# Performance work log

Measured on AMD Instinct MI355X. Metric: run time of the kernel, lower is better.

The kernel has to match this reference:

```python
import jax, jax.numpy as jnp
import numpy as np

N_SPK, N_UTT, D_EMB = 1024, 20, 512
COS_EPS = 1e-8   # torch F.cosine_similarity default eps
SIM_EPS = 1e-6   # added to cosine and inside the log, per original code


def setup_inputs() -> dict:
    key = jax.random.key(0)
    embeddings = jax.random.normal(key, (N_SPK, N_UTT, D_EMB), dtype=jnp.float32)
    w = jnp.asarray(10.0, dtype=jnp.float32)
    b = jnp.asarray(-5.0, dtype=jnp.float32)
    return {"embeddings": embeddings, "w": w, "b": b}


def reference(embeddings, w, b):
    N, M, D = embeddings.shape
    sums = embeddings.sum(axis=1)                       # [N, D]
    centroids = sums / M                                # [N, D] full centroids
    cent_excl = (sums[:, None, :] - embeddings) / (M - 1)  # [N, M, D] leave-one-out

    def _norm(x):
        return x / jnp.maximum(jnp.linalg.norm(x, axis=-1, keepdims=True), COS_EPS)

    e_n = _norm(embeddings)          # [N, M, D]
    c_n = _norm(centroids)           # [N, D]
    ce_n = _norm(cent_excl)          # [N, M, D]

    # cosine vs every speaker centroid
    cs = jnp.einsum('nmd,kd->nmk', e_n, c_n)            # [N, M, N]
    # replace same-speaker column with leave-one-out cosine
    diag = jnp.sum(e_n * ce_n, axis=-1)                 # [N, M]
    same = jnp.eye(N, dtype=bool)[:, None, :]           # [N, 1, N]
    cossim = jnp.where(same, diag[:, :, None], cs) + SIM_EPS

    sim = w * cossim + b                                # [N, M, N]
    pos = w * (diag + SIM_EPS) + b                      # sim[j, i, j]
    lse = jnp.log(jnp.sum(jnp.exp(sim), axis=-1) + SIM_EPS)  # [N, M]
    loss = jnp.sum(lse - pos)
    return loss
```

## Files before the change

### kernel.cpp

```cpp
#include <hip/hip_runtime.h>
#include <hip/hip_bf16.h>

typedef unsigned short u16;
typedef unsigned int u32;
typedef __bf16 bf16x8 __attribute__((ext_vector_type(8)));
typedef float f32x4 __attribute__((ext_vector_type(4)));

#define NSPK 1024
#define NUTT 20
#define DEMB 512
#define NROW (NSPK * NUTT)

__device__ __forceinline__ u16 f2bf(float x) {
    union { float f; u32 u; } v; v.f = x;
    u32 r = (v.u + 0x7fffu + ((v.u >> 16) & 1u)) >> 16;
    return (u16)r;
}

__global__ __launch_bounds__(256) void prep_f(const float* __restrict__ E,
                                              u16* __restrict__ A,
                                              u16* __restrict__ Bc,
                                              float* __restrict__ diag,
                                              float* __restrict__ csd,
                                              float* __restrict__ rs,
                                              float* __restrict__ out) {
    __shared__ float sbuf[4][DEMB];
    const int t = threadIdx.x, lane = t & 63, wv = t >> 6;
    const int n = blockIdx.x;
    const float* Eb = E + (size_t)n * (NUTT * DEMB) + (size_t)(wv * 5) * DEMB + lane * 8;

    float4 e0[5], e1[5];
    float4 p0 = {0, 0, 0, 0}, p1 = {0, 0, 0, 0};
#pragma unroll
    for (int i = 0; i < 5; ++i) {
        e0[i] = *(const float4*)(Eb + (size_t)i * DEMB);
        e1[i] = *(const float4*)(Eb + (size_t)i * DEMB + 4);
        p0.x += e0[i].x; p0.y += e0[i].y; p0.z += e0[i].z; p0.w += e0[i].w;
        p1.x += e1[i].x; p1.y += e1[i].y; p1.z += e1[i].z; p1.w += e1[i].w;
    }
    *(float4*)(&sbuf[wv][lane * 8])     = p0;
    *(float4*)(&sbuf[wv][lane * 8 + 4]) = p1;
    __syncthreads();

    float4 s0 = {0, 0, 0, 0}, s1 = {0, 0, 0, 0};
#pragma unroll
    for (int k = 0; k < 4; ++k) {
        float4 a = *(const float4*)(&sbuf[k][lane * 8]);
        float4 b = *(const float4*)(&sbuf[k][lane * 8 + 4]);
        s0.x += a.x; s0.y += a.y; s0.z += a.z; s0.w += a.w;
        s1.x += b.x; s1.y += b.y; s1.z += b.z; s1.w += b.w;
    }

    float ls = s0.x*s0.x + s0.y*s0.y + s0.z*s0.z + s0.w*s0.w
             + s1.x*s1.x + s1.y*s1.y + s1.z*s1.z + s1.w*s1.w;
#pragma unroll
    for (int o = 32; o; o >>= 1) ls += __shfl_xor(ls, o);
    const float ss = ls;
    const float rc = 1.0f / fmaxf(sqrtf(ss) * 0.05f, 1e-8f);
    const float g  = rc * 0.05f;

    union { u16 h[8]; uint4 q; } ck;
    ck.h[0] = f2bf(s0.x * g); ck.h[1] = f2bf(s0.y * g);
    ck.h[2] = f2bf(s0.z * g); ck.h[3] = f2bf(s0.w * g);
    ck.h[4] = f2bf(s1.x * g); ck.h[5] = f2bf(s1.y * g);
    ck.h[6] = f2bf(s1.z * g); ck.h[7] = f2bf(s1.w * g);
    ((uint4*)(Bc + (size_t)n * DEMB))[lane] = ck.q;

#pragma unroll
    for (int i = 0; i < 5; ++i) {
        float ee = e0[i].x*e0[i].x + e0[i].y*e0[i].y + e0[i].z*e0[i].z + e0[i].w*e0[i].w
                 + e1[i].x*e1[i].x + e1[i].y*e1[i].y + e1[i].z*e1[i].z + e1[i].w*e1[i].w;
        float es = e0[i].x*s0.x + e0[i].y*s0.y + e0[i].z*s0.z + e0[i].w*s0.w
                 + e1[i].x*s1.x + e1[i].y*s1.y + e1[i].z*s1.z + e1[i].w*s1.w;
#pragma unroll
        for (int o = 32; o; o >>= 1) { ee += __shfl_xor(ee, o); es += __shfl_xor(es, o); }

        const float rne = 1.0f / fmaxf(sqrtf(ee), 1e-8f);
        const float pxx = ss - 2.f * es + ee;
        const float dg  = (es - ee) * rne / fmaxf(sqrtf(pxx), 1.9e-7f);

        const int r = n * NUTT + wv * 5 + i;
        union { u16 h[8]; uint4 q; } pk;
        pk.h[0] = f2bf(e0[i].x * rne); pk.h[1] = f2bf(e0[i].y * rne);
        pk.h[2] = f2bf(e0[i].z * rne); pk.h[3] = f2bf(e0[i].w * rne);
        pk.h[4] = f2bf(e1[i].x * rne); pk.h[5] = f2bf(e1[i].y * rne);
        pk.h[6] = f2bf(e1[i].z * rne); pk.h[7] = f2bf(e1[i].w * rne);
        ((uint4*)(A + (size_t)r * DEMB))[lane] = pk.q;
        if (lane == 0) {
            diag[r] = dg;
            csd[r]  = es * g * rne;
        }
    }

    if (t < NUTT) rs[n * NUTT + t] = 0.f;
    if (n == 0 && t == 0) out[0] = 0.f;
}

__device__ __forceinline__ void async_copy16(const void* g, void* l) {
    __builtin_amdgcn_global_load_lds(
        (const __attribute__((address_space(1))) void*)g,
        (__attribute__((address_space(3))) void*)l, 16, 0, 0);
}

__global__ __launch_bounds__(256) void gemm_exp(const u16* __restrict__ A,
                                                const u16* __restrict__ Bc,
                                                const float* __restrict__ wp,
                                                const float* __restrict__ bp,
                                                float* __restrict__ rowsum) {
    __shared__ u16 As[128 * 64];
    __shared__ u16 Bs[128 * 64];
    const int t = threadIdx.x;
    const int lane = t & 63, wv = t >> 6;
    const int ml = lane & 15, q = lane >> 4;
    const int wm = wv >> 1, wn = wv & 1;
    const int tileM = blockIdx.x;
    const int tileN = blockIdx.y;

    const float w = *wp, bb = *bp;

    const u16* Ag = A + (size_t)tileM * 128 * DEMB;
    const u16* Bg = Bc + (size_t)tileN * 128 * DEMB;

    const u16* asrc[4]; const u16* bsrc[4]; u16* adst[4]; u16* bdst[4];
#pragma unroll
    for (int j = 0; j < 4; ++j) {
        const int c = t + 256 * j;
        const int r = c >> 3, kg = (c & 7) ^ (r & 7);
        asrc[j] = Ag + (size_t)r * DEMB + kg * 8;  adst[j] = As + c * 8;
        bsrc[j] = Bg + (size_t)r * DEMB + kg * 8;  bdst[j] = Bs + c * 8;
    }

    int aoff[2][4], boff[2][4];
#pragma unroll
    for (int i = 0; i < 4; ++i) {
        const int r = wm * 64 + i * 16 + ml;
        const int c = wn * 64 + i * 16 + ml;
#pragma unroll
        for (int h = 0; h < 2; ++h) {
            aoff[h][i] = r * 64 + ((((h << 2) | q) ^ (r & 7)) << 3);
            boff[h][i] = c * 64 + ((((h << 2) | q) ^ (c & 7)) << 3);
        }
    }

    f32x4 acc[4][4];
#pragma unroll
    for (int i = 0; i < 4; ++i)
#pragma unroll
        for (int j = 0; j < 4; ++j) acc[i][j] = (f32x4){0.f, 0.f, 0.f, 0.f};

    for (int kt = 0; kt < DEMB; kt += 64) {
        __syncthreads();
#pragma unroll
        for (int j = 0; j < 4; ++j) async_copy16(asrc[j] + kt, adst[j]);
#pragma unroll
        for (int j = 0; j < 4; ++j) async_copy16(bsrc[j] + kt, bdst[j]);
        __syncthreads();

#pragma unroll
        for (int h = 0; h < 2; ++h) {
            bf16x8 af[4], bfv[4];
#pragma unroll
            for (int i = 0; i < 4; ++i) af[i]  = *(const bf16x8*)(As + aoff[h][i]);
#pragma unroll
            for (int j = 0; j < 4; ++j) bfv[j] = *(const bf16x8*)(Bs + boff[h][j]);
#pragma unroll
            for (int i = 0; i < 4; ++i)
#pragma unroll
                for (int j = 0; j < 4; ++j)
                    acc[i][j] = __builtin_amdgcn_mfma_f32_16x16x32_bf16(af[i], bfv[j], acc[i][j], 0, 0, 0);
        }
    }

#pragma unroll
    for (int i = 0; i < 4; ++i) {
        float s0 = 0.f, s1 = 0.f, s2 = 0.f, s3 = 0.f;
#pragma unroll
        for (int j = 0; j < 4; ++j) {
            s0 += __expf(fmaf(w, acc[i][j][0] + 1e-6f, bb));
            s1 += __expf(fmaf(w, acc[i][j][1] + 1e-6f, bb));
            s2 += __expf(fmaf(w, acc[i][j][2] + 1e-6f, bb));
            s3 += __expf(fmaf(w, acc[i][j][3] + 1e-6f, bb));
        }
#pragma unroll
        for (int o = 1; o < 16; o <<= 1) {
            s0 += __shfl_xor(s0, o); s1 += __shfl_xor(s1, o);
            s2 += __shfl_xor(s2, o); s3 += __shfl_xor(s3, o);
        }
        if (ml < 4) {
            float sv = (ml == 0) ? s0 : (ml == 1) ? s1 : (ml == 2) ? s2 : s3;
            int grow = tileM * 128 + wm * 64 + i * 16 + q * 4 + ml;
            atomicAdd(&rowsum[grow], sv);
        }
    }
}

__global__ __launch_bounds__(256) void finalize(const float* __restrict__ rowsum,
                                                const float* __restrict__ diag,
                                                const float* __restrict__ csd,
                                                const float* __restrict__ wp,
                                                const float* __restrict__ bp,
                                                float* __restrict__ out) {
    __shared__ float s_red[4];
    const int r = blockIdx.x * 256 + threadIdx.x;
    const float w = *wp, bb = *bp;
    const float dg = diag[r];
    const float pos = fmaf(w, dg + 1e-6f, bb);
    const float S = rowsum[r] - __expf(fmaf(w, csd[r] + 1e-6f, bb)) + __expf(pos);
    float term = logf(S + 1e-6f) - pos;
    const int lane = threadIdx.x & 63, wv = threadIdx.x >> 6;
#pragma unroll
    for (int o = 32; o; o >>= 1) term += __shfl_xor(term, o);
    if (lane == 0) s_red[wv] = term;
    __syncthreads();
    if (threadIdx.x == 0) atomicAdd(out, s_red[0] + s_red[1] + s_red[2] + s_red[3]);
}

extern "C" void kernel_launch(void* const* d_in, const int* in_sizes, int n_in,
                              void* d_out, int out_size, void* d_ws, size_t ws_size,
                              hipStream_t stream) {
    const float* E = (const float*)d_in[0];
    const float* wp = (const float*)d_in[1];
    const float* bp = (const float*)d_in[2];
    float* out = (float*)d_out;

    char* ws = (char*)d_ws;
    u16* A     = (u16*)(ws);
    u16* Bc    = (u16*)(ws + 20971520);
    float* dg  = (float*)(ws + 22020096);
    float* cs  = (float*)(ws + 22102016);
    float* rs  = (float*)(ws + 22183936);

    prep_f<<<NSPK, 256, 0, stream>>>(E, A, Bc, dg, cs, rs, out);
    gemm_exp<<<dim3(160, 8), 256, 0, stream>>>(A, Bc, wp, bp, rs);
    finalize<<<80, 256, 0, stream>>>(rs, dg, cs, wp, bp, out);
}
```

Baseline: 120.9 us.

## Switch similarity GEMM from bf16 to fp8 using scaled MFMA 16x16x128

Normalized embeddings and centroids are now quantized to fp8 instead of bf16, and the GEMM uses the MI355X scaled fp8 MFMA with a K=128 tile and unit scales. The goal is to halve the bytes written and loaded for A and B and to reach the higher fp8 matrix throughput. LDS tiles, swizzle offsets and workspace offsets are adjusted to match. The cost is much lower precision in the cosine values, which after scaling by w=10 and exponentiation may push the loss outside tolerance.

```diff
diff --git a/kernel.cpp b/kernel.cpp
--- a/kernel.cpp
+++ b/kernel.cpp
@@ -3,7 +3,8 @@
 
 typedef unsigned short u16;
 typedef unsigned int u32;
-typedef __bf16 bf16x8 __attribute__((ext_vector_type(8)));
+typedef unsigned char u8;
+typedef int i32x8 __attribute__((ext_vector_type(8)));
 typedef float f32x4 __attribute__((ext_vector_type(4)));
 
 #define NSPK 1024
@@ -11,15 +12,18 @@
 #define DEMB 512
 #define NROW (NSPK * NUTT)
 
-__device__ __forceinline__ u16 f2bf(float x) {
-    union { float f; u32 u; } v; v.f = x;
-    u32 r = (v.u + 0x7fffu + ((v.u >> 16) & 1u)) >> 16;
-    return (u16)r;
+__device__ __forceinline__ uint2 pk_fp8x8(float a, float b, float c, float d,
+                                          float e, float f, float g, float h) {
+    int lo = __builtin_amdgcn_cvt_pk_fp8_f32(a, b, 0, 0);
+    lo = __builtin_amdgcn_cvt_pk_fp8_f32(c, d, lo, 1);
+    int hi = __builtin_amdgcn_cvt_pk_fp8_f32(e, f, 0, 0);
+    hi = __builtin_amdgcn_cvt_pk_fp8_f32(g, h, hi, 1);
+    return make_uint2((u32)lo, (u32)hi);
 }
 
 __global__ __launch_bounds__(256) void prep_f(const float* __restrict__ E,
-                                              u16* __restrict__ A,
-                                              u16* __restrict__ Bc,
+                                              u8* __restrict__ A,
+                                              u8* __restrict__ Bc,
                                               float* __restrict__ diag,
                                               float* __restrict__ csd,
                                               float* __restrict__ rs,
@@ -59,12 +63,9 @@
     const float rc = 1.0f / fmaxf(sqrtf(ss) * 0.05f, 1e-8f);
     const float g  = rc * 0.05f;
 
-    union { u16 h[8]; uint4 q; } ck;
-    ck.h[0] = f2bf(s0.x * g); ck.h[1] = f2bf(s0.y * g);
-    ck.h[2] = f2bf(s0.z * g); ck.h[3] = f2bf(s0.w * g);
-    ck.h[4] = f2bf(s1.x * g); ck.h[5] = f2bf(s1.y * g);
-    ck.h[6] = f2bf(s1.z * g); ck.h[7] = f2bf(s1.w * g);
-    ((uint4*)(Bc + (size_t)n * DEMB))[lane] = ck.q;
+    ((uint2*)(Bc + (size_t)n * DEMB))[lane] =
+        pk_fp8x8(s0.x * g, s0.y * g, s0.z * g, s0.w * g,
+                 s1.x * g, s1.y * g, s1.z * g, s1.w * g);
 
 #pragma unroll
     for (int i = 0; i < 5; ++i) {
@@ -80,12 +81,9 @@
         const float dg  = (es - ee) * rne / fmaxf(sqrtf(pxx), 1.9e-7f);
 
         const int r = n * NUTT + wv * 5 + i;
-        union { u16 h[8]; uint4 q; } pk;
-        pk.h[0] = f2bf(e0[i].x * rne); pk.h[1] = f2bf(e0[i].y * rne);
-        pk.h[2] = f2bf(e0[i].z * rne); pk.h[3] = f2bf(e0[i].w * rne);
-        pk.h[4] = f2bf(e1[i].x * rne); pk.h[5] = f2bf(e1[i].y * rne);
-        pk.h[6] = f2bf(e1[i].z * rne); pk.h[7] = f2bf(e1[i].w * rne);
-        ((uint4*)(A + (size_t)r * DEMB))[lane] = pk.q;
+        ((uint2*)(A + (size_t)r * DEMB))[lane] =
+            pk_fp8x8(e0[i].x * rne, e0[i].y * rne, e0[i].z * rne, e0[i].w * rne,
+                     e1[i].x * rne, e1[i].y * rne, e1[i].z * rne, e1[i].w * rne);
         if (lane == 0) {
             diag[r] = dg;
             csd[r]  = es * g * rne;
@@ -102,13 +100,13 @@
         (__attribute__((address_space(3))) void*)l, 16, 0, 0);
 }
 
-__global__ __launch_bounds__(256) void gemm_exp(const u16* __restrict__ A,
-                                                const u16* __restrict__ Bc,
-                                                const float* __restrict__ wp,
-                                                const float* __restrict__ bp,
-                                                float* __restrict__ rowsum) {
-    __shared__ u16 As[128 * 64];
-    __shared__ u16 Bs[128 * 64];
+__global__ __launch_bounds__(256) void gemm_mx(const u8* __restrict__ A,
+                                               const u8* __restrict__ Bc,
+                                               const float* __restrict__ wp,
+                                               const float* __restrict__ bp,
+                                               float* __restrict__ rowsum) {
+    __shared__ u8 As[128 * 128];
+    __shared__ u8 Bs[128 * 128];
     const int t = threadIdx.x;
     const int lane = t & 63, wv = t >> 6;
     const int ml = lane & 15, q = lane >> 4;
@@ -118,28 +116,27 @@
 
     const float w = *wp, bb = *bp;
 
-    const u16* Ag = A + (size_t)tileM * 128 * DEMB;
-    const u16* Bg = Bc + (size_t)tileN * 128 * DEMB;
-
-    const u16* asrc[4]; const u16* bsrc[4]; u16* adst[4]; u16* bdst[4];
+    const u8* Ag = A + (size_t)tileM * 128 * DEMB;
+    const u8* Bg = Bc + (size_t)tileN * 128 * DEMB;
+
+    const u8* asrc[4]; const u8* bsrc[4]; u8* adst[4]; u8* bdst[4];
 #pragma unroll
     for (int j = 0; j < 4; ++j) {
         const int c = t + 256 * j;
         const int r = c >> 3, kg = (c & 7) ^ (r & 7);
-        asrc[j] = Ag + (size_t)r * DEMB + kg * 8;  adst[j] = As + c * 8;
-        bsrc[j] = Bg + (size_t)r * DEMB + kg * 8;  bdst[j] = Bs + c * 8;
-    }
-
-    int aoff[2][4], boff[2][4];
+        asrc[j] = Ag + (size_t)r * DEMB + kg * 16;  adst[j] = As + c * 16;
+        bsrc[j] = Bg + (size_t)r * DEMB + kg * 16;  bdst[j] = Bs + c * 16;
+    }
+
+    int a0[4], a1[4], b0[4], b1[4];
 #pragma unroll
     for (int i = 0; i < 4; ++i) {
         const int r = wm * 64 + i * 16 + ml;
         const int c = wn * 64 + i * 16 + ml;
-#pragma unroll
-        for (int h = 0; h < 2; ++h) {
-            aoff[h][i] = r * 64 + ((((h << 2) | q) ^ (r & 7)) << 3);
-            boff[h][i] = c * 64 + ((((h << 2) | q) ^ (c & 7)) << 3);
-        }
+        a0[i] = r * 128 + (((2 * q)     ^ (r & 7)) << 4);
+        a1[i] = r * 128 + (((2 * q + 1) ^ (r & 7)) << 4);
+        b0[i] = c * 128 + (((2 * q)     ^ (c & 7)) << 4);
+        b1[i] = c * 128 + (((2 * q + 1) ^ (c & 7)) << 4);
     }
 
     f32x4 acc[4][4];
@@ -148,7 +145,7 @@
 #pragma unroll
         for (int j = 0; j < 4; ++j) acc[i][j] = (f32x4){0.f, 0.f, 0.f, 0.f};
 
-    for (int kt = 0; kt < DEMB; kt += 64) {
+    for (int kt = 0; kt < DEMB; kt += 128) {
         __syncthreads();
 #pragma unroll
         for (int j = 0; j < 4; ++j) async_copy16(asrc[j] + kt, adst[j]);
@@ -156,19 +153,28 @@
         for (int j = 0; j < 4; ++j) async_copy16(bsrc[j] + kt, bdst[j]);
         __syncthreads();
 
-#pragma unroll
-        for (int h = 0; h < 2; ++h) {
-            bf16x8 af[4], bfv[4];
-#pragma unroll
-            for (int i = 0; i < 4; ++i) af[i]  = *(const bf16x8*)(As + aoff[h][i]);
-#pragma unroll
-            for (int j = 0; j < 4; ++j) bfv[j] = *(const bf16x8*)(Bs + boff[h][j]);
-#pragma unroll
-            for (int i = 0; i < 4; ++i)
-#pragma unroll
-                for (int j = 0; j < 4; ++j)
-                    acc[i][j] = __builtin_amdgcn_mfma_f32_16x16x32_bf16(af[i], bfv[j], acc[i][j], 0, 0, 0);
-        }
+        i32x8 af[4], bf[4];
+#pragma unroll
+        for (int i = 0; i < 4; ++i) {
+            uint4 x = *(const uint4*)(As + a0[i]);
+            uint4 y = *(const uint4*)(As + a1[i]);
+            af[i] = (i32x8){(int)x.x, (int)x.y, (int)x.z, (int)x.w,
+                            (int)y.x, (int)y.y, (int)y.z, (int)y.w};
+        }
+#pragma unroll
+        for (int j = 0; j < 4; ++j) {
+            uint4 x = *(const uint4*)(Bs + b0[j]);
+            uint4 y = *(const uint4*)(Bs + b1[j]);
+            bf[j] = (i32x8){(int)x.x, (int)x.y, (int)x.z, (int)x.w,
+                            (int)y.x, (int)y.y, (int)y.z, (int)y.w};
+        }
+#pragma unroll
+        for (int i = 0; i < 4; ++i)
+#pragma unroll
+            for (int j = 0; j < 4; ++j)
+                acc[i][j] = __builtin_amdgcn_mfma_scale_f32_16x16x128_f8f6f4(
+                    af[i], bf[j], acc[i][j], 0, 0,
+                    0, 0x7F7F7F7F, 0, 0x7F7F7F7F);
     }
 
 #pragma unroll
@@ -224,13 +230,13 @@
     float* out = (float*)d_out;
 
     char* ws = (char*)d_ws;
-    u16* A     = (u16*)(ws);
-    u16* Bc    = (u16*)(ws + 20971520);
-    float* dg  = (float*)(ws + 22020096);
-    float* cs  = (float*)(ws + 22102016);
-    float* rs  = (float*)(ws + 22183936);
+    u8* A      = (u8*)(ws);
+    u8* Bc     = (u8*)(ws + 10485760);
+    float* dg  = (float*)(ws + 11010048);
+    float* cs  = (float*)(ws + 11091968);
+    float* rs  = (float*)(ws + 11173888);
 
     prep_f<<<NSPK, 256, 0, stream>>>(E, A, Bc, dg, cs, rs, out);
-    gemm_exp<<<dim3(160, 8), 256, 0, stream>>>(A, Bc, wp, bp, rs);
+    gemm_mx<<<dim3(160, 8), 256, 0, stream>>>(A, Bc, wp, bp, rs);
     finalize<<<80, 256, 0, stream>>>(rs, dg, cs, wp, bp, out);
 }
```

New measurement: 109.6 us. 1.1x faster.
